# Kernel tuning notes

Measured on AMD Instinct MI355X. Metric: run time of the kernel, lower is better.

## Reference

```python
import jax, jax.numpy as jnp
import numpy as np

NT = 32          # nt_states
T = 64           # t_states
ST = NT + T      # total states
NEG = -1e9       # matches self.huge fill


def setup_inputs() -> dict:
    key = jax.random.key(0)
    k1, k2, k3 = jax.random.split(key, 3)
    B, n = 8, 28
    return {
        "unary_scores": jax.random.normal(k1, (B, n, T), dtype=jnp.float32),
        "rule_scores": jax.random.normal(k2, (B, NT, ST, ST), dtype=jnp.float32),
        "root_scores": jax.random.normal(k3, (B, NT), dtype=jnp.float32),
    }


def _inside(unary_scores, rule_scores, root_scores):
    # Chart indexed beta[b, width, start, state]; span (s, s+w) lives at [b, w, s].
    # Invalid (state-range) slots hold NEG, so exp() underflows them to exactly 0,
    # reproducing the terminal/nonterminal slice logic of the torch code.
    B, n, _ = unary_scores.shape
    beta = jnp.full((B, n, n, ST), NEG, dtype=unary_scores.dtype)
    beta = beta.at[:, 0, :, NT:].set(unary_scores)  # width-0 diagonal: preterminals

    mrule = rule_scores.max(axis=(2, 3))                    # [B, A]
    erule = jnp.exp(rule_scores - mrule[:, :, None, None])  # [B, A, L, R]

    for w in range(1, n):
        S = n - w                     # number of valid start positions
        k = np.arange(w)              # split offset: u = s + k
        # left child: span (s, s+k) -> width k, start s
        left = beta[:, :w, :S, :]                                  # [B, w, S, ST]
        # right child: span (s+k+1, s+w) -> width w-1-k, start s+k+1
        sr = k[:, None] + 1 + np.arange(S)[None, :]                # [w, S]
        right = beta[:, (w - 1 - k)[:, None], sr, :]               # [B, w, S, ST]

        # stable logsumexp over (k, l, r) via exp-space matmuls
        ml = left.max(-1)                                          # [B, w, S]
        mr = right.max(-1)                                         # [B, w, S]
        M = (ml + mr).max(1)                                       # [B, S]
        el = jnp.exp(left - ml[..., None])
        er = jnp.exp(right - mr[..., None] + (ml + mr - M[:, None, :])[..., None])
        numer = jnp.einsum('bksl,bksr->bslr', el, er)              # [B, S, L, R]
        total = jnp.einsum('bslr,balr->bsa', numer, erule)         # [B, S, A]
        score = jnp.log(total) + M[..., None] + mrule[:, None, :]
        beta = beta.at[:, w, :S, :NT].set(score)

    top = beta[:, n - 1, 0, :NT] + root_scores                     # span (0, n-1)
    return jax.nn.logsumexp(top, axis=1)                           # log Z, [B]


def reference(unary_scores, rule_scores, root_scores):
    return _inside(unary_scores, rule_scores, root_scores)
```

## Files before the change

kernel.cpp:

```cpp
#include <hip/hip_runtime.h>
#include <cstdint>
#include <cstddef>


#define NMAX 28
#define SLOTT 864
#define SLOTN 3456

#define R_ELT 0
#define R_F   1856
#define R_G   5568
#define R_F2  9280
#define R_G2  12992
#define R_TRI 16704
#define R_BMX 22736
#define R_ENA 23520
#define C_TRI 0
#define C_BMX 6032
#define C_GPP 6816
#define C_ELK 7584
#define C_ERK 8608
#define C_NUM 14752
#define C_RED 16536
#define LDSF  27616

__device__ __forceinline__ int off32(int w, int n) {
    return (w - 1) * n - (w * (w - 1)) / 2;
}
__device__ __forceinline__ float gload(const float* p) {
    return __hip_atomic_load(p, __ATOMIC_RELAXED, __HIP_MEMORY_SCOPE_AGENT);
}
__device__ __forceinline__ void gstore(float* p, float v) {
    __hip_atomic_store(p, v, __ATOMIC_RELAXED, __HIP_MEMORY_SCOPE_AGENT);
}
__device__ __forceinline__ unsigned gloadu(const unsigned* p) {
    return __hip_atomic_load(p, __ATOMIC_RELAXED, __HIP_MEMORY_SCOPE_AGENT);
}
__device__ __forceinline__ void gstoreu(unsigned* p, unsigned v) {
    __hip_atomic_store(p, v, __ATOMIC_RELAXED, __HIP_MEMORY_SCOPE_AGENT);
}
__device__ __forceinline__ float dot4acc(float4 m, float4 t, float acc) {
    return fmaf(m.x, t.x, fmaf(m.y, t.y, fmaf(m.z, t.z, fmaf(m.w, t.w, acc))));
}
__device__ __forceinline__ float b2f(unsigned short u) {
    return __uint_as_float(((unsigned)u) << 16);
}
__device__ __forceinline__ unsigned short f2b(float x) {
    unsigned u = __float_as_uint(x);
    return (unsigned short)((u + 0x7fffu + ((u >> 16) & 1u)) >> 16);
}
__device__ __forceinline__ float maxM(const float* bmx, int w, int s) {
    float M = -3.0e38f;
    for (int k = 0; k < w; ++k)
        M = fmaxf(M, bmx[k * NMAX + s] + bmx[(w - 1 - k) * NMAX + s + k + 1]);
    return M;
}
__device__ __forceinline__ float maxMc(const float* bmx, int w, int s) {
    float M = -3.0e38f;
    for (int k = 2; k <= w - 3; ++k)
        M = fmaxf(M, bmx[k * NMAX + s] + bmx[(w - 1 - k) * NMAX + s + k + 1]);
    return M;
}
__device__ __forceinline__ void finalize_row(float* lds, int triOff, int bmxOff,
                                             const float* slot, int wf, int n,
                                             int tid) {
    int Sp = n - wf;
    if (tid < Sp * 32) {
        int s = tid >> 5, aa = tid & 31;
        float q = gload(slot + s * 32 + aa);
        float m2 = q;
        for (int off = 16; off > 0; off >>= 1)
            m2 = fmaxf(m2, __shfl_xor(m2, off, 32));
        ((unsigned short*)(lds + triOff))[(off32(wf, n) + s) * 32 + aa] = f2b(q / m2);
        if (aa == 0)
            lds[bmxOff + wf * NMAX + s] = __logf(m2) + maxM(lds + bmxOff, wf, s);
    }
}

__global__ __launch_bounds__(256) void prep_kernel(const float* __restrict__ unary,
                                                   float* __restrict__ elT_g,
                                                   float* __restrict__ bmax0_g,
                                                   unsigned* __restrict__ flags,
                                                   int n) {
    int b = blockIdx.x, tid = threadIdx.x;
    if (tid < 16) gstoreu(&flags[b * 32 + tid], (tid >= 8) ? 4u : 0u);
    for (int pos = tid >> 6; pos < n; pos += 4) {
        int t = tid & 63;
        float v = unary[((size_t)(b * n) + pos) * 64 + t];
        float m = v;
        for (int off = 32; off > 0; off >>= 1) m = fmaxf(m, __shfl_xor(m, off, 64));
        elT_g[(size_t)b * 64 * n + t * n + pos] = __expf(v - m);
        if (t == 0) bmax0_g[b * 32 + pos] = m;
    }
}

__global__ __launch_bounds__(256) void pack_kernel(const float* __restrict__ rule,
                                                   const float* __restrict__ elT_g,
                                                   float* __restrict__ H_g,
                                                   float* __restrict__ F_g,
                                                   float* __restrict__ G_g,
                                                   float* __restrict__ ENa_g,
                                                   float* __restrict__ ENc_g,
                                                   int n) {
    extern __shared__ float sl[];
    int b = blockIdx.y, aa = blockIdx.x, tid = threadIdx.x;
    const int ag = aa >> 2, a4 = aa & 3;
    const float4* rs4 = (const float4*)(rule + (size_t)(b * 32 + aa) * 9216);
    for (int i = tid; i < 2304; i += 256) {
        float4 v = rs4[i];
        float4 o;
        o.x = __expf(v.x); o.y = __expf(v.y); o.z = __expf(v.z); o.w = __expf(v.w);
        ((float4*)sl)[i] = o;
    }
    for (int i = tid; i < 64 * n; i += 256)
        sl[9216 + i] = elT_g[(size_t)b * 64 * n + i];
    __syncthreads();
    const float* elt = sl + 9216;
    if (tid < 256) {
        int flat = tid * 4, l = flat >> 5, r = flat & 31;
        float4 o = *(const float4*)(sl + l * 96 + r);
        *(float4*)(ENc_g + ((size_t)(b * 256 + tid) * 32 + aa) * 4) = o;
    }
    for (int i = tid; i < 1024; i += 256)
        ENa_g[((size_t)(b * 8 + ag) * 4096) + a4 * 1024 + i] = sl[(i >> 5) * 96 + (i & 31)];
    for (int i = tid; i < 64 * n; i += 256) {
        int r = i / n, s = i - r * n;
        float acc = 0.f;
        for (int l = 0; l < 64; ++l)
            acc = fmaf(elt[l * n + s], sl[(32 + l) * 96 + 32 + r], acc);
        H_g[(size_t)(b * 8 + ag) * 7424 + (r * 29 + s) * 4 + a4] = acc;
    }
    for (int i = tid; i < 32 * n; i += 256) {
        int r = i / n, s = i - r * n;
        float acc = 0.f;
        for (int l = 0; l < 64; ++l)
            acc = fmaf(elt[l * n + s], sl[(32 + l) * 96 + r], acc);
        F_g[(size_t)(b * 8 + ag) * 3712 + (r * 29 + s) * 4 + a4] = acc;
    }
    for (int i = tid; i < 32 * n; i += 256) {
        int l = i / n, s = i - l * n;
        float acc = 0.f;
        for (int r = 0; r < 64; ++r)
            acc = fmaf(elt[r * n + s], sl[l * 96 + 32 + r], acc);
        G_g[(size_t)(b * 8 + ag) * 3712 + (l * 29 + s) * 4 + a4] = acc;
    }
}

__global__ __launch_bounds__(1024, 1) void inside_kernel(
    const float* __restrict__ elT_g, const float* __restrict__ bmax0_g,
    const float* __restrict__ H_g, const float* __restrict__ F_g,
    const float* __restrict__ G_g, const float* __restrict__ ENa_g,
    const float* __restrict__ ENc_g,
    float* __restrict__ ringT, float* __restrict__ ringN,
    const float* __restrict__ root, float* __restrict__ out,
    unsigned* __restrict__ flags, int n) {
    extern __shared__ float lds[];
    const int b = blockIdx.x >> 4, ch = blockIdx.x & 15;
    const int tid = threadIdx.x;
    unsigned* const fl = flags + b * 32;
    float* const rT = ringT + (size_t)b * 8 * SLOTT;
    float* const rN = ringN + (size_t)b * 4 * SLOTN;

    if (ch < 8) {
        for (int i = tid; i < 64 * n; i += 1024) {
            int t = i / n, pos = i - t * n;
            lds[R_ELT + t * 29 + pos] = elT_g[(size_t)b * 64 * n + i];
        }
        for (int i = tid; i < 3712; i += 1024) lds[R_F + i] = F_g[(size_t)(b * 8 + ch) * 3712 + i];
        for (int i = tid; i < 3712; i += 1024) lds[R_G + i] = G_g[(size_t)(b * 8 + ch) * 3712 + i];
        for (int i = tid; i < 7424; i += 1024) lds[R_F2 + i] = H_g[(size_t)(b * 8 + ch) * 7424 + i];
        for (int i = tid; i < 4096; i += 1024) lds[R_ENA + i] = ENa_g[(size_t)(b * 8 + ch) * 4096 + i];
        if (tid < n) lds[R_BMX + tid] = bmax0_g[b * 32 + tid];
        __syncthreads();

        for (int w = 1; w < n; ++w) {
            const int S = n - w;
            if (tid < 64) {
                unsigned tgt = 0u;
                if (tid < 8) tgt = (w >= 2) ? (unsigned)(w - 1) : 0u;
                else if (tid < 16 && w >= 5) {
                    int p = (tid - 8) >> 2;
                    if (p == (w & 1)) tgt = (unsigned)w;
                }
                for (;;) {
                    unsigned v = (tid < 16) ? gloadu(&fl[tid]) : 0u;
                    if (__ballot(v < tgt) == 0ull) break;
                    __builtin_amdgcn_s_sleep(1);
                }
            }
            __syncthreads();

            if (w >= 2)
                finalize_row(lds, R_TRI, R_BMX, rT + (size_t)((w - 1) & 7) * SLOTT,
                             w - 1, n, tid);
            __syncthreads();

            if (w == 2) {
                const unsigned short* tri = (const unsigned short*)(lds + R_TRI);
                const int b1 = off32(1, n);
                for (int i = tid; i < 32 * 29 * 4; i += 1024) {
                    int a4 = i & 3, rest = i >> 2, s = rest % 29, rl = rest / 29;
                    if (s < n - 1) {
                        float accF = 0.f, accG = 0.f;
                        for (int q = 0; q < 32; ++q) {
                            float e1 = b2f(tri[(b1 + s) * 32 + q]);
                            accF = fmaf(e1, lds[R_ENA + a4 * 1024 + q * 32 + rl], accF);
                            accG = fmaf(lds[R_ENA + a4 * 1024 + rl * 32 + q], e1, accG);
                        }
                        lds[R_F2 + (rl * 29 + s) * 4 + a4] = accF;
                        lds[R_G2 + (rl * 29 + s) * 4 + a4] = accG;
                    }
                }
                __syncthreads();
            }

            if (tid < S * 4) {
                int s = tid >> 2, a4 = tid & 3, a = ch * 4 + a4;
                float cr0 = 0.f, cr1 = 0.f, cr2 = 0.f, cr3 = 0.f;
                if (w >= 5) {
                    const float* p = rN + (size_t)(w & 3) * SLOTN + (size_t)(s * 32 + a) * 4;
                    cr0 = gload(p); cr1 = gload(p + 1); cr2 = gload(p + 2); cr3 = gload(p + 3);
                }
                float M = maxM(lds + R_BMX, w, s);
                const unsigned short* tri = (const unsigned short*)(lds + R_TRI);
                float t2;
                if (w == 1) {
                    float acc = 0.f;
                    for (int r = 0; r < 64; ++r)
                        acc = fmaf(lds[R_ELT + r * 29 + s + 1],
                                   lds[R_F2 + (r * 29 + s) * 4 + a4], acc);
                    t2 = acc;
                } else {
                    int b1 = off32(w - 1, n);
                    float aTN = 0.f, aNT = 0.f;
                    for (int r = 0; r < 32; ++r)
                        aTN = fmaf(b2f(tri[(b1 + s + 1) * 32 + r]),
                                   lds[R_F + (r * 29 + s) * 4 + a4], aTN);
                    for (int l = 0; l < 32; ++l)
                        aNT = fmaf(b2f(tri[(b1 + s) * 32 + l]),
                                   lds[R_G + (l * 29 + s + w) * 4 + a4], aNT);
                    float g0 = __expf(lds[R_BMX + s] + lds[R_BMX + (w - 1) * NMAX + s + 1] - M);
                    float gw = __expf(lds[R_BMX + (w - 1) * NMAX + s] + lds[R_BMX + s + w] - M);
                    t2 = aTN * g0 + aNT * gw;
                    if (w >= 3) {
                        int b2 = off32(w - 2, n);
                        float e1 = 0.f;
                        for (int r = 0; r < 32; ++r)
                            e1 = fmaf(b2f(tri[(b2 + s + 2) * 32 + r]),
                                      lds[R_F2 + (r * 29 + s) * 4 + a4], e1);
                        t2 = fmaf(e1, __expf(lds[R_BMX + NMAX + s] +
                                             lds[R_BMX + (w - 2) * NMAX + s + 2] - M), t2);
                        if (w >= 4) {
                            float e2 = 0.f;
                            for (int l = 0; l < 32; ++l)
                                e2 = fmaf(b2f(tri[(b2 + s) * 32 + l]),
                                          lds[R_G2 + (l * 29 + s + w - 1) * 4 + a4], e2);
                            t2 = fmaf(e2, __expf(lds[R_BMX + (w - 2) * NMAX + s] +
                                                 lds[R_BMX + NMAX + s + w - 1] - M), t2);
                        }
                    }
                    if (w >= 5) {
                        float Mc = maxMc(lds + R_BMX, w, s);
                        t2 = fmaf(((cr0 + cr1) + (cr2 + cr3)), __expf(Mc - M), t2);
                    }
                }
                gstore(rT + (size_t)(w & 7) * SLOTT + s * 32 + a, t2);
            }
            __syncthreads();
            if (tid == 0) gstoreu(&fl[ch], (unsigned)w);
        }

        if (ch == 0) {
            if (tid < 64) {
                unsigned tgt = (unsigned)(n - 1);
                for (;;) {
                    unsigned v = (tid < 8) ? gloadu(&fl[tid]) : tgt;
                    if (__ballot(v < tgt) == 0ull) break;
                    __builtin_amdgcn_s_sleep(1);
                }
            }
            __syncthreads();
            if (tid < 32) {
                float q = gload(rT + (size_t)((n - 1) & 7) * SLOTT + tid);
                float v = q * __expf(root[b * 32 + tid]);
                for (int off = 16; off > 0; off >>= 1) v += __shfl_xor(v, off, 32);
                if (tid == 0) out[b] = maxM(lds + R_BMX, n - 1, 0) + __logf(v);
            }
        }
    } else {
        const int idx = ch - 8, slice = idx & 3, par = idx >> 2;
        float4 e4;
        {
            int g = tid >> 5, a = tid & 31;
            e4 = *(const float4*)(ENc_g + ((size_t)(b * 256 + slice * 32 + g) * 32 + a) * 4);
        }
        if (tid < n) lds[C_BMX + tid] = bmax0_g[b * 32 + tid];
        __syncthreads();
        int lastFin = 0;
        const int W0 = (par == 1) ? 5 : 6;
        for (int W = W0; W < n; W += 2) {
            const int S = n - W, Sp2 = S | 1;
            const int cnt = W - 4;
            int q4 = (cnt + 3) >> 2; if (!(q4 & 1)) ++q4;
            const int K4 = 4 * q4;
            if (tid < 64) {
                unsigned tgt = (unsigned)(W - 3);
                for (;;) {
                    unsigned v = (tid < 8) ? gloadu(&fl[tid]) : tgt;
                    if (__ballot(v < tgt) == 0ull) break;
                    __builtin_amdgcn_s_sleep(1);
                }
            }
            __syncthreads();
            for (int wf = lastFin + 1; wf <= W - 3; ++wf) {
                finalize_row(lds, C_TRI, C_BMX, rT + (size_t)(wf & 7) * SLOTT, wf, n, tid);
                __syncthreads();
            }
            lastFin = W - 3;
            if (tid < cnt * 32) {
                int k = (tid >> 5) + 2, s = tid & 31;
                if (s < S) {
                    float Mc = maxMc(lds + C_BMX, W, s);
                    lds[C_GPP + (k - 2) * 32 + s] =
                        __expf(lds[C_BMX + k * NMAX + s] +
                               lds[C_BMX + (W - 1 - k) * NMAX + s + k + 1] - Mc);
                }
            }
            __syncthreads();
            if (tid < S * 32) {
                int s = tid >> 5, sym = tid & 31;
                const unsigned short* tri = (const unsigned short*)(lds + C_TRI);
                int eo = (sym * Sp2 + s) * K4;
                for (int k = 2; k <= W - 3; ++k)
                    lds[C_ERK + eo + k - 2] =
                        b2f(tri[(off32(W - 1 - k, n) + s + k + 1) * 32 + sym]) *
                        lds[C_GPP + (k - 2) * 32 + s];
                for (int j = cnt; j < K4; ++j) lds[C_ERK + eo + j] = 0.f;
                if (sym < 4) {
                    int lo = (sym * Sp2 + s) * K4;
                    int gl = slice * 4 + sym;
                    for (int k = 2; k <= W - 3; ++k)
                        lds[C_ELK + lo + k - 2] = b2f(tri[(off32(k, n) + s) * 32 + gl]);
                    for (int j = cnt; j < K4; ++j) lds[C_ELK + lo + j] = 0.f;
                }
            }
            __syncthreads();
            {
                int cL = tid & 127, sh = tid >> 7;
                int lloc = cL >> 5, r = cL & 31;
                unsigned short* np = (unsigned short*)(lds + C_NUM);
                for (int s = sh; s < S; s += 8) {
                    const float* ep = lds + C_ELK + (lloc * Sp2 + s) * K4;
                    const float* rp = lds + C_ERK + (r * Sp2 + s) * K4;
                    float acc = 0.f;
                    for (int j = 0; j < K4; j += 4)
                        acc = dot4acc(*(const float4*)(ep + j), *(const float4*)(rp + j), acc);
                    np[s * 132 + cL] = f2b(acc);
                }
            }
            __syncthreads();
            {
                const unsigned short* np = (const unsigned short*)(lds + C_NUM);
                unsigned short* red = (unsigned short*)(lds + C_RED);
                int g = tid >> 5, a = tid & 31, wv = tid >> 6;
                bool low = (tid & 32) == 0;
                for (int s = 0; s < S; ++s) {
                    const unsigned short* pp = np + s * 132 + g * 4;
                    float acc = b2f(pp[0]) * e4.x + b2f(pp[1]) * e4.y +
                                b2f(pp[2]) * e4.z + b2f(pp[3]) * e4.w;
                    acc += __shfl_xor(acc, 32, 64);
                    if (low) red[wv * 896 + s * 32 + a] = f2b(acc);
                }
            }
            __syncthreads();
            if (tid < S * 32) {
                const unsigned short* red = (const unsigned short*)(lds + C_RED);
                float t = 0.f;
                for (int g2 = 0; g2 < 16; ++g2) t += b2f(red[g2 * 896 + tid]);
                gstore(rN + (size_t)(W & 3) * SLOTN + (size_t)tid * 4 + slice, t);
            }
            __syncthreads();
            if (tid == 0) gstoreu(&fl[ch], (unsigned)W);
        }
    }
}

extern "C" void kernel_launch(void* const* d_in, const int* in_sizes, int n_in,
                              void* d_out, int out_size, void* d_ws, size_t ws_size,
                              hipStream_t stream) {
    const float* unary = (const float*)d_in[0];
    const float* rule  = (const float*)d_in[1];
    const float* root  = (const float*)d_in[2];
    float* out = (float*)d_out;

    const int B = in_sizes[2] / 32;
    int n = in_sizes[0] / (B * 64);

    float* ws = (float*)d_ws;
    float* elT_g = ws;
    float* bmax0 = elT_g + (size_t)B * 64 * n;
    float* H_g   = bmax0 + (size_t)B * 32;
    float* F_g   = H_g + (size_t)B * 8 * 7424;
    float* G_g   = F_g + (size_t)B * 8 * 3712;
    float* ENa_g = G_g + (size_t)B * 8 * 3712;
    float* ENc_g = ENa_g + (size_t)B * 8 * 4096;
    float* ringT = ENc_g + (size_t)B * 32768;
    float* ringN = ringT + (size_t)B * 8 * SLOTT;
    unsigned* flags = (unsigned*)(ringN + (size_t)B * 4 * SLOTN);

    prep_kernel<<<dim3(B), 256, 0, stream>>>(unary, elT_g, bmax0, flags, n);

    const int packLds = (9216 + 64 * n) * 4;
    hipFuncSetAttribute((const void*)pack_kernel,
                        hipFuncAttributeMaxDynamicSharedMemorySize, packLds);
    pack_kernel<<<dim3(32, B), 256, packLds, stream>>>(rule, elT_g, H_g, F_g,
                                                       G_g, ENa_g, ENc_g, n);

    hipFuncSetAttribute((const void*)inside_kernel,
                        hipFuncAttributeMaxDynamicSharedMemorySize, LDSF * 4);
    void* args[] = {
        (void*)&elT_g, (void*)&bmax0, (void*)&H_g, (void*)&F_g, (void*)&G_g,
        (void*)&ENa_g, (void*)&ENc_g, (void*)&ringT, (void*)&ringN,
        (void*)&root, (void*)&out, (void*)&flags, (void*)&n
    };
    hipLaunchCooperativeKernel((void*)inside_kernel, dim3(B * 16), dim3(1024),
                               args, LDSF * 4, stream);
}
```

Measured before the change: 260.8 us.

## Restructure inside pass into row worker plus eight table/contraction blocks per batch

Reorganizes the persistent cooperative kernel from 16 blocks per batch to 9. One row worker block computes each chart row from precomputed per-split folded rule tables for the four outermost split pairs on each side. The other blocks build those tables and compute the central splits' contraction in fp32 LDS instead of bf16. The pack kernel now precomputes the width-1 row and the F/G terminal tables directly, and the row worker prefetches central-split partials from a ring buffer. The aim is to cut per-row synchronization latency on the serial critical path, at the cost of more global table traffic, a larger LDS footprint and a more complex flag protocol.

```diff
diff --git a/kernel.cpp b/kernel.cpp
--- a/kernel.cpp
+++ b/kernel.cpp
@@ -4,25 +4,20 @@
 
 
 #define NMAX 28
-#define SLOTT 864
-#define SLOTN 3456
-
-#define R_ELT 0
-#define R_F   1856
-#define R_G   5568
-#define R_F2  9280
-#define R_G2  12992
-#define R_TRI 16704
-#define R_BMX 22736
-#define R_ENA 23520
-#define C_TRI 0
-#define C_BMX 6032
-#define C_GPP 6816
-#define C_ELK 7584
-#define C_ERK 8608
-#define C_NUM 14752
-#define C_RED 16536
-#define LDSF  27616
+#define RT_SLOT 896
+#define RN_SLOT 1728
+#define TABSZ 28672
+
+#define RW_TRI 0
+#define RW_BMX 12096
+#define RW_CB  12880
+#define CO_TRI 0
+#define CO_BMX 12096
+#define CO_ELK 12880
+#define CO_ERK 16144
+#define CO_NUM 22672
+#define CO_RED 28132
+#define LDSF   35300
 
 __device__ __forceinline__ int off32(int w, int n) {
     return (w - 1) * n - (w * (w - 1)) / 2;
@@ -38,9 +33,6 @@
 }
 __device__ __forceinline__ void gstoreu(unsigned* p, unsigned v) {
     __hip_atomic_store(p, v, __ATOMIC_RELAXED, __HIP_MEMORY_SCOPE_AGENT);
-}
-__device__ __forceinline__ float dot4acc(float4 m, float4 t, float acc) {
-    return fmaf(m.x, t.x, fmaf(m.y, t.y, fmaf(m.z, t.z, fmaf(m.w, t.w, acc))));
 }
 __device__ __forceinline__ float b2f(unsigned short u) {
     return __uint_as_float(((unsigned)u) << 16);
@@ -55,26 +47,22 @@
         M = fmaxf(M, bmx[k * NMAX + s] + bmx[(w - 1 - k) * NMAX + s + k + 1]);
     return M;
 }
-__device__ __forceinline__ float maxMc(const float* bmx, int w, int s) {
+__device__ __forceinline__ float maxMc4(const float* bmx, int w, int s) {
     float M = -3.0e38f;
-    for (int k = 2; k <= w - 3; ++k)
+    for (int k = 4; k <= w - 5; ++k)
         M = fmaxf(M, bmx[k * NMAX + s] + bmx[(w - 1 - k) * NMAX + s + k + 1]);
     return M;
 }
-__device__ __forceinline__ void finalize_row(float* lds, int triOff, int bmxOff,
-                                             const float* slot, int wf, int n,
-                                             int tid) {
-    int Sp = n - wf;
-    if (tid < Sp * 32) {
-        int s = tid >> 5, aa = tid & 31;
-        float q = gload(slot + s * 32 + aa);
-        float m2 = q;
-        for (int off = 16; off > 0; off >>= 1)
-            m2 = fmaxf(m2, __shfl_xor(m2, off, 32));
-        ((unsigned short*)(lds + triOff))[(off32(wf, n) + s) * 32 + aa] = f2b(q / m2);
-        if (aa == 0)
-            lds[bmxOff + wf * NMAX + s] = __logf(m2) + maxM(lds + bmxOff, wf, s);
-    }
+__device__ __forceinline__ float dot32(const float* tri, const float* tab) {
+    float acc = 0.f;
+    #pragma unroll
+    for (int j = 0; j < 8; ++j) {
+        float4 tv = *(const float4*)(tri + j * 4);
+        float4 fv = *(const float4*)(tab + j * 4);
+        acc = fmaf(tv.x, fv.x, acc); acc = fmaf(tv.y, fv.y, acc);
+        acc = fmaf(tv.z, fv.z, acc); acc = fmaf(tv.w, fv.w, acc);
+    }
+    return acc;
 }
 
 __global__ __launch_bounds__(256) void prep_kernel(const float* __restrict__ unary,
@@ -83,7 +71,7 @@
                                                    unsigned* __restrict__ flags,
                                                    int n) {
     int b = blockIdx.x, tid = threadIdx.x;
-    if (tid < 16) gstoreu(&flags[b * 32 + tid], (tid >= 8) ? 4u : 0u);
+    if (tid < 32) gstoreu(&flags[b * 32 + tid], 0u);
     for (int pos = tid >> 6; pos < n; pos += 4) {
         int t = tid & 63;
         float v = unary[((size_t)(b * n) + pos) * 64 + t];
@@ -96,15 +84,15 @@
 
 __global__ __launch_bounds__(256) void pack_kernel(const float* __restrict__ rule,
                                                    const float* __restrict__ elT_g,
-                                                   float* __restrict__ H_g,
-                                                   float* __restrict__ F_g,
-                                                   float* __restrict__ G_g,
+                                                   float* __restrict__ T1_g,
+                                                   float* __restrict__ Ftab,
+                                                   float* __restrict__ Gtab,
                                                    float* __restrict__ ENa_g,
+                                                   float* __restrict__ ENb_g,
                                                    float* __restrict__ ENc_g,
                                                    int n) {
-    extern __shared__ float sl[];
+    __shared__ float sl[11008];
     int b = blockIdx.y, aa = blockIdx.x, tid = threadIdx.x;
-    const int ag = aa >> 2, a4 = aa & 3;
     const float4* rs4 = (const float4*)(rule + (size_t)(b * 32 + aa) * 9216);
     for (int i = tid; i < 2304; i += 256) {
         float4 v = rs4[i];
@@ -116,271 +104,330 @@
         sl[9216 + i] = elT_g[(size_t)b * 64 * n + i];
     __syncthreads();
     const float* elt = sl + 9216;
+    if (tid < (n - 1) * 8) {
+        int s = tid >> 3, sub = tid & 7;
+        float acc = 0.f;
+        for (int l = sub * 8; l < sub * 8 + 8; ++l) {
+            float el = elt[l * n + s];
+            const float* row = sl + (32 + l) * 96 + 32;
+            float inner = 0.f;
+            for (int r = 0; r < 64; ++r)
+                inner = fmaf(elt[r * n + s + 1], row[r], inner);
+            acc = fmaf(el, inner, acc);
+        }
+        acc += __shfl_xor(acc, 1, 8);
+        acc += __shfl_xor(acc, 2, 8);
+        acc += __shfl_xor(acc, 4, 8);
+        if (sub == 0) T1_g[(size_t)b * 864 + s * 32 + aa] = acc;
+    }
+    for (int i = tid; i < 32 * n; i += 256) {
+        int r = i & 31, s = i >> 5;
+        float acc = 0.f;
+        for (int l = 0; l < 64; ++l)
+            acc = fmaf(elt[l * n + s], sl[(32 + l) * 96 + r], acc);
+        Ftab[(size_t)b * TABSZ + (s * 32 + aa) * 32 + r] = acc;
+    }
+    for (int i = tid; i < 32 * n; i += 256) {
+        int l = i & 31, s = i >> 5;
+        float acc = 0.f;
+        for (int r = 0; r < 64; ++r)
+            acc = fmaf(elt[r * n + s], sl[l * 96 + 32 + r], acc);
+        Gtab[(size_t)b * TABSZ + (s * 32 + aa) * 32 + l] = acc;
+    }
+    for (int i = tid; i < 1024; i += 256) {
+        ENa_g[(size_t)b * 32768 + aa * 1024 + i] = sl[(i >> 5) * 96 + (i & 31)];
+        ENb_g[(size_t)b * 32768 + aa * 1024 + i] = sl[(i & 31) * 96 + (i >> 5)];
+    }
     if (tid < 256) {
         int flat = tid * 4, l = flat >> 5, r = flat & 31;
         float4 o = *(const float4*)(sl + l * 96 + r);
         *(float4*)(ENc_g + ((size_t)(b * 256 + tid) * 32 + aa) * 4) = o;
     }
-    for (int i = tid; i < 1024; i += 256)
-        ENa_g[((size_t)(b * 8 + ag) * 4096) + a4 * 1024 + i] = sl[(i >> 5) * 96 + (i & 31)];
-    for (int i = tid; i < 64 * n; i += 256) {
-        int r = i / n, s = i - r * n;
-        float acc = 0.f;
-        for (int l = 0; l < 64; ++l)
-            acc = fmaf(elt[l * n + s], sl[(32 + l) * 96 + 32 + r], acc);
-        H_g[(size_t)(b * 8 + ag) * 7424 + (r * 29 + s) * 4 + a4] = acc;
-    }
-    for (int i = tid; i < 32 * n; i += 256) {
-        int r = i / n, s = i - r * n;
-        float acc = 0.f;
-        for (int l = 0; l < 64; ++l)
-            acc = fmaf(elt[l * n + s], sl[(32 + l) * 96 + r], acc);
-        F_g[(size_t)(b * 8 + ag) * 3712 + (r * 29 + s) * 4 + a4] = acc;
-    }
-    for (int i = tid; i < 32 * n; i += 256) {
-        int l = i / n, s = i - l * n;
-        float acc = 0.f;
-        for (int r = 0; r < 64; ++r)
-            acc = fmaf(elt[r * n + s], sl[l * 96 + 32 + r], acc);
-        G_g[(size_t)(b * 8 + ag) * 3712 + (l * 29 + s) * 4 + a4] = acc;
-    }
 }
 
 __global__ __launch_bounds__(1024, 1) void inside_kernel(
-    const float* __restrict__ elT_g, const float* __restrict__ bmax0_g,
-    const float* __restrict__ H_g, const float* __restrict__ F_g,
-    const float* __restrict__ G_g, const float* __restrict__ ENa_g,
-    const float* __restrict__ ENc_g,
+    const float* __restrict__ T1_g, const float* __restrict__ bmax0_g,
+    float* __restrict__ tabs, const float* __restrict__ ENa_g,
+    const float* __restrict__ ENb_g, const float* __restrict__ ENc_g,
     float* __restrict__ ringT, float* __restrict__ ringN,
     const float* __restrict__ root, float* __restrict__ out,
-    unsigned* __restrict__ flags, int n) {
+    unsigned* __restrict__ flags, int n, int B) {
     extern __shared__ float lds[];
-    const int b = blockIdx.x >> 4, ch = blockIdx.x & 15;
+    const int b = blockIdx.x / 9, r9 = blockIdx.x % 9;
     const int tid = threadIdx.x;
     unsigned* const fl = flags + b * 32;
-    float* const rT = ringT + (size_t)b * 8 * SLOTT;
-    float* const rN = ringN + (size_t)b * 4 * SLOTN;
-
-    if (ch < 8) {
-        for (int i = tid; i < 64 * n; i += 1024) {
-            int t = i / n, pos = i - t * n;
-            lds[R_ELT + t * 29 + pos] = elT_g[(size_t)b * 64 * n + i];
-        }
-        for (int i = tid; i < 3712; i += 1024) lds[R_F + i] = F_g[(size_t)(b * 8 + ch) * 3712 + i];
-        for (int i = tid; i < 3712; i += 1024) lds[R_G + i] = G_g[(size_t)(b * 8 + ch) * 3712 + i];
-        for (int i = tid; i < 7424; i += 1024) lds[R_F2 + i] = H_g[(size_t)(b * 8 + ch) * 7424 + i];
-        for (int i = tid; i < 4096; i += 1024) lds[R_ENA + i] = ENa_g[(size_t)(b * 8 + ch) * 4096 + i];
-        if (tid < n) lds[R_BMX + tid] = bmax0_g[b * 32 + tid];
+    float* const rT = ringT + (size_t)b * 8 * RT_SLOT;
+    float* const rN = ringN + (size_t)b * 4 * RN_SLOT;
+    const size_t tb = (size_t)b * TABSZ;
+    const size_t tstep = (size_t)B * TABSZ;
+
+    if (r9 == 0) {
+        if (tid < n) lds[RW_BMX + tid] = bmax0_g[b * 32 + tid];
         __syncthreads();
 
         for (int w = 1; w < n; ++w) {
             const int S = n - w;
+            if (w >= 3 && w <= 8) {
+                if (tid < 64) {
+                    while (gloadu(fl + 16 + (w - 3)) < 1u)
+                        __builtin_amdgcn_s_sleep(8);
+                }
+                __syncthreads();
+            }
+
+            if (tid < S * 32) {
+                const int s = tid >> 5, a = tid & 31;
+                float Mloc = 0.f, t2;
+                if (w == 1) {
+                    t2 = T1_g[(size_t)b * 864 + tid];
+                    if (a == 0) Mloc = maxM(lds + RW_BMX, 1, s);
+                } else {
+                    float gv = 0.f;
+                    if (a < 9) {
+                        Mloc = maxM(lds + RW_BMX, w, s);
+                        const float* B_ = lds + RW_BMX;
+                        float x = -3.0e38f;
+                        if      (a == 0) x = B_[s] + B_[(w - 1) * NMAX + s + 1];
+                        else if (a == 1) x = B_[(w - 1) * NMAX + s] + B_[s + w];
+                        else if (a == 2 && w >= 3) x = B_[NMAX + s] + B_[(w - 2) * NMAX + s + 2];
+                        else if (a == 3 && w >= 4) x = B_[(w - 2) * NMAX + s] + B_[NMAX + s + w - 1];
+                        else if (a == 4 && w >= 5) x = B_[2 * NMAX + s] + B_[(w - 3) * NMAX + s + 3];
+                        else if (a == 5 && w >= 6) x = B_[(w - 3) * NMAX + s] + B_[2 * NMAX + s + w - 2];
+                        else if (a == 6 && w >= 7) x = B_[3 * NMAX + s] + B_[(w - 4) * NMAX + s + 4];
+                        else if (a == 7 && w >= 8) x = B_[(w - 4) * NMAX + s] + B_[3 * NMAX + s + w - 3];
+                        else if (a == 8 && w >= 9) x = maxMc4(B_, w, s);
+                        gv = (x > -1.0e38f) ? __expf(x - Mloc) : 0.f;
+                    }
+                    float g0 = __shfl(gv, 0, 32), gw = __shfl(gv, 1, 32);
+                    float g1 = __shfl(gv, 2, 32), g2x = __shfl(gv, 3, 32);
+                    float g3 = __shfl(gv, 4, 32), g3x = __shfl(gv, 5, 32);
+                    float g4 = __shfl(gv, 6, 32), g4x = __shfl(gv, 7, 32);
+                    float gc = __shfl(gv, 8, 32);
+                    const float* TRIp = lds + RW_TRI;
+                    const size_t ca = (size_t)(s * 32 + a) * 32;
+                    t2 = g0 * dot32(TRIp + (off32(w - 1, n) + s + 1) * 32,
+                                    tabs + 0 * tstep + tb + ca)
+                       + gw * dot32(TRIp + (off32(w - 1, n) + s) * 32,
+                                    tabs + 1 * tstep + tb + (size_t)((s + w) * 32 + a) * 32);
+                    if (w >= 3)
+                        t2 = fmaf(g1, dot32(TRIp + (off32(w - 2, n) + s + 2) * 32,
+                                            tabs + 2 * tstep + tb + ca), t2);
+                    if (w >= 4)
+                        t2 = fmaf(g2x, dot32(TRIp + (off32(w - 2, n) + s) * 32,
+                                             tabs + 3 * tstep + tb + (size_t)((s + w - 1) * 32 + a) * 32), t2);
+                    if (w >= 5)
+                        t2 = fmaf(g3, dot32(TRIp + (off32(w - 3, n) + s + 3) * 32,
+                                            tabs + 4 * tstep + tb + ca), t2);
+                    if (w >= 6)
+                        t2 = fmaf(g3x, dot32(TRIp + (off32(w - 3, n) + s) * 32,
+                                             tabs + 5 * tstep + tb + (size_t)((s + w - 2) * 32 + a) * 32), t2);
+                    if (w >= 7)
+                        t2 = fmaf(g4, dot32(TRIp + (off32(w - 4, n) + s + 4) * 32,
+                                            tabs + 6 * tstep + tb + ca), t2);
+                    if (w >= 8)
+                        t2 = fmaf(g4x, dot32(TRIp + (off32(w - 4, n) + s) * 32,
+                                             tabs + 7 * tstep + tb + (size_t)((s + w - 3) * 32 + a) * 32), t2);
+                    if (w >= 9)
+                        t2 = fmaf(gc, lds[RW_CB + (w & 1) * 864 + tid], t2);
+                }
+                float m2 = t2;
+                for (int off = 16; off > 0; off >>= 1)
+                    m2 = fmaxf(m2, __shfl_xor(m2, off, 32));
+                float eB = t2 / m2;
+                lds[RW_TRI + (off32(w, n) + s) * 32 + a] = eB;
+                gstore(rT + (size_t)(w & 7) * RT_SLOT + tid, eB);
+                if (a == 0) {
+                    float bm = __logf(m2) + Mloc;
+                    lds[RW_BMX + w * NMAX + s] = bm;
+                    gstore(rT + (size_t)(w & 7) * RT_SLOT + 864 + s, bm);
+                }
+            } else if (tid >= 896) {
+                const int wn = w + 1;
+                if (wn >= 9 && wn < n) {
+                    const int grp = wn & 3, pre = tid - 896;
+                    const unsigned* f0 = fl + 8 + grp * 2;
+                    for (;;) {
+                        if (gloadu(f0) >= (unsigned)wn && gloadu(f0 + 1) >= (unsigned)wn)
+                            break;
+                        __builtin_amdgcn_s_sleep(8);
+                    }
+                    const int Sn = n - wn;
+                    const float* src = rN + (size_t)(wn & 3) * RN_SLOT;
+                    for (int e = pre; e < Sn * 32; e += 128)
+                        lds[RW_CB + (wn & 1) * 864 + e] =
+                            gload(src + e * 2) + gload(src + e * 2 + 1);
+                }
+            }
+            __syncthreads();
+            if (tid == 0) gstoreu(fl, (unsigned)w);
+        }
+
+        if (tid < 32) {
+            float eB = lds[RW_TRI + off32(n - 1, n) * 32 + tid];
+            float v = eB * __expf(root[b * 32 + tid]);
+            for (int off = 16; off > 0; off >>= 1) v += __shfl_xor(v, off, 32);
+            if (tid == 0) out[b] = lds[RW_BMX + (n - 1) * NMAX] + __logf(v);
+        }
+    } else {
+        const int idx = r9 - 1, grp = idx >> 1, sl = idx & 1;
+        int tableId = -1;
+        if (idx == 0) tableId = 0; else if (idx == 1) tableId = 1;
+        else if (idx == 6) tableId = 2; else if (idx == 7) tableId = 3;
+        else if (idx == 4) tableId = 4; else if (idx == 5) tableId = 5;
+
+        if (tableId >= 0) {
+            const int foldRow = 1 + (tableId >> 1);
+            const bool isF = (tableId & 1) == 0;
             if (tid < 64) {
-                unsigned tgt = 0u;
-                if (tid < 8) tgt = (w >= 2) ? (unsigned)(w - 1) : 0u;
-                else if (tid < 16 && w >= 5) {
-                    int p = (tid - 8) >> 2;
-                    if (p == (w & 1)) tgt = (unsigned)w;
-                }
-                for (;;) {
-                    unsigned v = (tid < 16) ? gloadu(&fl[tid]) : 0u;
-                    if (__ballot(v < tgt) == 0ull) break;
-                    __builtin_amdgcn_s_sleep(1);
-                }
-            }
-            __syncthreads();
-
-            if (w >= 2)
-                finalize_row(lds, R_TRI, R_BMX, rT + (size_t)((w - 1) & 7) * SLOTT,
-                             w - 1, n, tid);
-            __syncthreads();
-
-            if (w == 2) {
-                const unsigned short* tri = (const unsigned short*)(lds + R_TRI);
-                const int b1 = off32(1, n);
-                for (int i = tid; i < 32 * 29 * 4; i += 1024) {
-                    int a4 = i & 3, rest = i >> 2, s = rest % 29, rl = rest / 29;
-                    if (s < n - 1) {
-                        float accF = 0.f, accG = 0.f;
-                        for (int q = 0; q < 32; ++q) {
-                            float e1 = b2f(tri[(b1 + s) * 32 + q]);
-                            accF = fmaf(e1, lds[R_ENA + a4 * 1024 + q * 32 + rl], accF);
-                            accG = fmaf(lds[R_ENA + a4 * 1024 + rl * 32 + q], e1, accG);
-                        }
-                        lds[R_F2 + (rl * 29 + s) * 4 + a4] = accF;
-                        lds[R_G2 + (rl * 29 + s) * 4 + a4] = accG;
+                while (gloadu(fl) < (unsigned)foldRow) __builtin_amdgcn_s_sleep(8);
+            }
+            __syncthreads();
+            const int cntE = (n - foldRow) * 32;
+            for (int e = tid; e < cntE; e += 1024)
+                lds[CO_TRI + e] = gload(rT + (size_t)(foldRow & 7) * RT_SLOT + e);
+            __syncthreads();
+            const int maxSx = n - foldRow;
+            if (tid < maxSx * 32) {
+                const int sx = tid >> 5, a = tid & 31;
+                const float* EN = (isF ? ENa_g : ENb_g) + (size_t)b * 32768 + a * 1024;
+                float4 acc[8];
+                #pragma unroll
+                for (int j = 0; j < 8; ++j) acc[j] = make_float4(0.f, 0.f, 0.f, 0.f);
+                for (int q = 0; q < 32; ++q) {
+                    float e = lds[CO_TRI + sx * 32 + q];
+                    const float4* ev = (const float4*)(EN + q * 32);
+                    #pragma unroll
+                    for (int j = 0; j < 8; ++j) {
+                        float4 v = ev[j];
+                        acc[j].x = fmaf(e, v.x, acc[j].x);
+                        acc[j].y = fmaf(e, v.y, acc[j].y);
+                        acc[j].z = fmaf(e, v.z, acc[j].z);
+                        acc[j].w = fmaf(e, v.w, acc[j].w);
                     }
                 }
-                __syncthreads();
-            }
-
-            if (tid < S * 4) {
-                int s = tid >> 2, a4 = tid & 3, a = ch * 4 + a4;
-                float cr0 = 0.f, cr1 = 0.f, cr2 = 0.f, cr3 = 0.f;
-                if (w >= 5) {
-                    const float* p = rN + (size_t)(w & 3) * SLOTN + (size_t)(s * 32 + a) * 4;
-                    cr0 = gload(p); cr1 = gload(p + 1); cr2 = gload(p + 2); cr3 = gload(p + 3);
-                }
-                float M = maxM(lds + R_BMX, w, s);
-                const unsigned short* tri = (const unsigned short*)(lds + R_TRI);
-                float t2;
-                if (w == 1) {
-                    float acc = 0.f;
-                    for (int r = 0; r < 64; ++r)
-                        acc = fmaf(lds[R_ELT + r * 29 + s + 1],
-                                   lds[R_F2 + (r * 29 + s) * 4 + a4], acc);
-                    t2 = acc;
-                } else {
-                    int b1 = off32(w - 1, n);
-                    float aTN = 0.f, aNT = 0.f;
-                    for (int r = 0; r < 32; ++r)
-                        aTN = fmaf(b2f(tri[(b1 + s + 1) * 32 + r]),
-                                   lds[R_F + (r * 29 + s) * 4 + a4], aTN);
-                    for (int l = 0; l < 32; ++l)
-                        aNT = fmaf(b2f(tri[(b1 + s) * 32 + l]),
-                                   lds[R_G + (l * 29 + s + w) * 4 + a4], aNT);
-                    float g0 = __expf(lds[R_BMX + s] + lds[R_BMX + (w - 1) * NMAX + s + 1] - M);
-                    float gw = __expf(lds[R_BMX + (w - 1) * NMAX + s] + lds[R_BMX + s + w] - M);
-                    t2 = aTN * g0 + aNT * gw;
-                    if (w >= 3) {
-                        int b2 = off32(w - 2, n);
-                        float e1 = 0.f;
-                        for (int r = 0; r < 32; ++r)
-                            e1 = fmaf(b2f(tri[(b2 + s + 2) * 32 + r]),
-                                      lds[R_F2 + (r * 29 + s) * 4 + a4], e1);
-                        t2 = fmaf(e1, __expf(lds[R_BMX + NMAX + s] +
-                                             lds[R_BMX + (w - 2) * NMAX + s + 2] - M), t2);
-                        if (w >= 4) {
-                            float e2 = 0.f;
-                            for (int l = 0; l < 32; ++l)
-                                e2 = fmaf(b2f(tri[(b2 + s) * 32 + l]),
-                                          lds[R_G2 + (l * 29 + s + w - 1) * 4 + a4], e2);
-                            t2 = fmaf(e2, __expf(lds[R_BMX + (w - 2) * NMAX + s] +
-                                                 lds[R_BMX + NMAX + s + w - 1] - M), t2);
-                        }
-                    }
-                    if (w >= 5) {
-                        float Mc = maxMc(lds + R_BMX, w, s);
-                        t2 = fmaf(((cr0 + cr1) + (cr2 + cr3)), __expf(Mc - M), t2);
-                    }
-                }
-                gstore(rT + (size_t)(w & 7) * SLOTT + s * 32 + a, t2);
-            }
-            __syncthreads();
-            if (tid == 0) gstoreu(&fl[ch], (unsigned)w);
-        }
-
-        if (ch == 0) {
-            if (tid < 64) {
-                unsigned tgt = (unsigned)(n - 1);
-                for (;;) {
-                    unsigned v = (tid < 8) ? gloadu(&fl[tid]) : tgt;
-                    if (__ballot(v < tgt) == 0ull) break;
-                    __builtin_amdgcn_s_sleep(1);
-                }
-            }
-            __syncthreads();
-            if (tid < 32) {
-                float q = gload(rT + (size_t)((n - 1) & 7) * SLOTT + tid);
-                float v = q * __expf(root[b * 32 + tid]);
-                for (int off = 16; off > 0; off >>= 1) v += __shfl_xor(v, off, 32);
-                if (tid == 0) out[b] = maxM(lds + R_BMX, n - 1, 0) + __logf(v);
-            }
-        }
-    } else {
-        const int idx = ch - 8, slice = idx & 3, par = idx >> 2;
-        float4 e4;
+                float* dp = tabs + (size_t)(2 + tableId) * tstep + tb +
+                            (size_t)(sx * 32 + a) * 32;
+                #pragma unroll
+                for (int j = 0; j < 8; ++j) {
+                    gstore(dp + j * 4 + 0, acc[j].x);
+                    gstore(dp + j * 4 + 1, acc[j].y);
+                    gstore(dp + j * 4 + 2, acc[j].z);
+                    gstore(dp + j * 4 + 3, acc[j].w);
+                }
+            }
+            __syncthreads();
+            if (tid == 0) gstoreu(fl + 16 + tableId, 1u);
+        }
+
+        float4 e4[4];
         {
             int g = tid >> 5, a = tid & 31;
-            e4 = *(const float4*)(ENc_g + ((size_t)(b * 256 + slice * 32 + g) * 32 + a) * 4);
-        }
-        if (tid < n) lds[C_BMX + tid] = bmax0_g[b * 32 + tid];
-        __syncthreads();
-        int lastFin = 0;
-        const int W0 = (par == 1) ? 5 : 6;
-        for (int W = W0; W < n; W += 2) {
+            #pragma unroll
+            for (int i = 0; i < 4; ++i)
+                e4[i] = *(const float4*)(ENc_g +
+                    ((size_t)(b * 256 + sl * 128 + g * 4 + i) * 32 + a) * 4);
+        }
+        int lastFin = 3;
+        const int W0 = (grp == 0) ? 12 : 8 + grp;
+        for (int W = W0; W < n; W += 4) {
             const int S = n - W, Sp2 = S | 1;
-            const int cnt = W - 4;
+            const int cnt = W - 8;
             int q4 = (cnt + 3) >> 2; if (!(q4 & 1)) ++q4;
             const int K4 = 4 * q4;
             if (tid < 64) {
-                unsigned tgt = (unsigned)(W - 3);
-                for (;;) {
-                    unsigned v = (tid < 8) ? gloadu(&fl[tid]) : tgt;
-                    if (__ballot(v < tgt) == 0ull) break;
-                    __builtin_amdgcn_s_sleep(1);
-                }
-            }
-            __syncthreads();
-            for (int wf = lastFin + 1; wf <= W - 3; ++wf) {
-                finalize_row(lds, C_TRI, C_BMX, rT + (size_t)(wf & 7) * SLOTT, wf, n, tid);
-                __syncthreads();
-            }
-            lastFin = W - 3;
-            if (tid < cnt * 32) {
-                int k = (tid >> 5) + 2, s = tid & 31;
-                if (s < S) {
-                    float Mc = maxMc(lds + C_BMX, W, s);
-                    lds[C_GPP + (k - 2) * 32 + s] =
-                        __expf(lds[C_BMX + k * NMAX + s] +
-                               lds[C_BMX + (W - 1 - k) * NMAX + s + k + 1] - Mc);
-                }
+                while (gloadu(fl) < (unsigned)(W - 5)) __builtin_amdgcn_s_sleep(8);
+            }
+            __syncthreads();
+            {
+                const int nf = (W - 5) - lastFin;
+                float ev[4], bv[4];
+                for (int i = 0; i < nf; ++i) {
+                    int wf = lastFin + 1 + i;
+                    ev[i] = (tid < (n - wf) * 32)
+                        ? gload(rT + (size_t)(wf & 7) * RT_SLOT + tid) : 0.f;
+                    bv[i] = (tid < (n - wf))
+                        ? gload(rT + (size_t)(wf & 7) * RT_SLOT + 864 + tid) : 0.f;
+                }
+                for (int i = 0; i < nf; ++i) {
+                    int wf = lastFin + 1 + i;
+                    if (tid < (n - wf) * 32)
+                        lds[CO_TRI + (off32(wf, n) + (tid >> 5)) * 32 + (tid & 31)] = ev[i];
+                    if (tid < (n - wf)) lds[CO_BMX + wf * NMAX + tid] = bv[i];
+                }
+                lastFin = W - 5;
             }
             __syncthreads();
             if (tid < S * 32) {
                 int s = tid >> 5, sym = tid & 31;
-                const unsigned short* tri = (const unsigned short*)(lds + C_TRI);
+                float Mc = maxMc4(lds + CO_BMX, W, s);
                 int eo = (sym * Sp2 + s) * K4;
-                for (int k = 2; k <= W - 3; ++k)
-                    lds[C_ERK + eo + k - 2] =
-                        b2f(tri[(off32(W - 1 - k, n) + s + k + 1) * 32 + sym]) *
-                        lds[C_GPP + (k - 2) * 32 + s];
-                for (int j = cnt; j < K4; ++j) lds[C_ERK + eo + j] = 0.f;
-                if (sym < 4) {
+                for (int k = 4; k <= W - 5; ++k)
+                    lds[CO_ERK + eo + k - 4] =
+                        lds[CO_TRI + (off32(W - 1 - k, n) + s + k + 1) * 32 + sym] *
+                        __expf(lds[CO_BMX + k * NMAX + s] +
+                               lds[CO_BMX + (W - 1 - k) * NMAX + s + k + 1] - Mc);
+                for (int j = cnt; j < K4; ++j) lds[CO_ERK + eo + j] = 0.f;
+                if (sym < 16) {
                     int lo = (sym * Sp2 + s) * K4;
-                    int gl = slice * 4 + sym;
-                    for (int k = 2; k <= W - 3; ++k)
-                        lds[C_ELK + lo + k - 2] = b2f(tri[(off32(k, n) + s) * 32 + gl]);
-                    for (int j = cnt; j < K4; ++j) lds[C_ELK + lo + j] = 0.f;
+                    int gl = sl * 16 + sym;
+                    for (int k = 4; k <= W - 5; ++k)
+                        lds[CO_ELK + lo + k - 4] =
+                            lds[CO_TRI + (off32(k, n) + s) * 32 + gl];
+                    for (int j = cnt; j < K4; ++j) lds[CO_ELK + lo + j] = 0.f;
                 }
             }
             __syncthreads();
             {
-                int cL = tid & 127, sh = tid >> 7;
+                int cL = tid & 511, sh = tid >> 9;
                 int lloc = cL >> 5, r = cL & 31;
-                unsigned short* np = (unsigned short*)(lds + C_NUM);
-                for (int s = sh; s < S; s += 8) {
-                    const float* ep = lds + C_ELK + (lloc * Sp2 + s) * K4;
-                    const float* rp = lds + C_ERK + (r * Sp2 + s) * K4;
+                unsigned short* np = (unsigned short*)(lds + CO_NUM);
+                for (int s = sh; s < S; s += 2) {
+                    const float* ep = lds + CO_ELK + (lloc * Sp2 + s) * K4;
+                    const float* rp = lds + CO_ERK + (r * Sp2 + s) * K4;
                     float acc = 0.f;
-                    for (int j = 0; j < K4; j += 4)
-                        acc = dot4acc(*(const float4*)(ep + j), *(const float4*)(rp + j), acc);
-                    np[s * 132 + cL] = f2b(acc);
+                    for (int j = 0; j < K4; j += 4) {
+                        float4 a4 = *(const float4*)(ep + j);
+                        float4 b4 = *(const float4*)(rp + j);
+                        acc = fmaf(a4.x, b4.x, fmaf(a4.y, b4.y,
+                              fmaf(a4.z, b4.z, fmaf(a4.w, b4.w, acc))));
+                    }
+                    np[s * 520 + cL] = f2b(acc);
                 }
             }
             __syncthreads();
             {
-                const unsigned short* np = (const unsigned short*)(lds + C_NUM);
-                unsigned short* red = (unsigned short*)(lds + C_RED);
+                const char* nbase = (const char*)(lds + CO_NUM);
+                unsigned short* red = (unsigned short*)(lds + CO_RED);
                 int g = tid >> 5, a = tid & 31, wv = tid >> 6;
                 bool low = (tid & 32) == 0;
                 for (int s = 0; s < S; ++s) {
-                    const unsigned short* pp = np + s * 132 + g * 4;
-                    float acc = b2f(pp[0]) * e4.x + b2f(pp[1]) * e4.y +
-                                b2f(pp[2]) * e4.z + b2f(pp[3]) * e4.w;
+                    uint4 u0 = *(const uint4*)(nbase + s * 1040 + g * 32);
+                    uint4 u1 = *(const uint4*)(nbase + s * 1040 + g * 32 + 16);
+                    #define LOu(x) __uint_as_float((x) << 16)
+                    #define HIu(x) __uint_as_float((x) & 0xffff0000u)
+                    float acc = LOu(u0.x) * e4[0].x + HIu(u0.x) * e4[0].y
+                              + LOu(u0.y) * e4[0].z + HIu(u0.y) * e4[0].w
+                              + LOu(u0.z) * e4[1].x + HIu(u0.z) * e4[1].y
+                              + LOu(u0.w) * e4[1].z + HIu(u0.w) * e4[1].w
+                              + LOu(u1.x) * e4[2].x + HIu(u1.x) * e4[2].y
+                              + LOu(u1.y) * e4[2].z + HIu(u1.y) * e4[2].w
+                              + LOu(u1.z) * e4[3].x + HIu(u1.z) * e4[3].y
+                              + LOu(u1.w) * e4[3].z + HIu(u1.w) * e4[3].w;
+                    #undef LOu
+                    #undef HIu
                     acc += __shfl_xor(acc, 32, 64);
                     if (low) red[wv * 896 + s * 32 + a] = f2b(acc);
                 }
             }
             __syncthreads();
             if (tid < S * 32) {
-                const unsigned short* red = (const unsigned short*)(lds + C_RED);
+                const unsigned short* red = (const unsigned short*)(lds + CO_RED);
                 float t = 0.f;
                 for (int g2 = 0; g2 < 16; ++g2) t += b2f(red[g2 * 896 + tid]);
-                gstore(rN + (size_t)(W & 3) * SLOTN + (size_t)tid * 4 + slice, t);
-            }
-            __syncthreads();
-            if (tid == 0) gstoreu(&fl[ch], (unsigned)W);
+                gstore(rN + (size_t)(W & 3) * RN_SLOT + (size_t)tid * 2 + sl, t);
+            }
+            __syncthreads();
+            if (tid == 0) gstoreu(fl + 8 + grp * 2 + sl, (unsigned)W);
         }
     }
 }
@@ -399,30 +446,28 @@
     float* ws = (float*)d_ws;
     float* elT_g = ws;
     float* bmax0 = elT_g + (size_t)B * 64 * n;
-    float* H_g   = bmax0 + (size_t)B * 32;
-    float* F_g   = H_g + (size_t)B * 8 * 7424;
-    float* G_g   = F_g + (size_t)B * 8 * 3712;
-    float* ENa_g = G_g + (size_t)B * 8 * 3712;
-    float* ENc_g = ENa_g + (size_t)B * 8 * 4096;
+    float* T1_g  = bmax0 + (size_t)B * 32;
+    float* tabs  = T1_g + (size_t)B * 864;
+    float* ENa_g = tabs + (size_t)8 * B * TABSZ;
+    float* ENb_g = ENa_g + (size_t)B * 32768;
+    float* ENc_g = ENb_g + (size_t)B * 32768;
     float* ringT = ENc_g + (size_t)B * 32768;
-    float* ringN = ringT + (size_t)B * 8 * SLOTT;
-    unsigned* flags = (unsigned*)(ringN + (size_t)B * 4 * SLOTN);
+    float* ringN = ringT + (size_t)B * 8 * RT_SLOT;
+    unsigned* flags = (unsigned*)(ringN + (size_t)B * 4 * RN_SLOT);
 
     prep_kernel<<<dim3(B), 256, 0, stream>>>(unary, elT_g, bmax0, flags, n);
-
-    const int packLds = (9216 + 64 * n) * 4;
-    hipFuncSetAttribute((const void*)pack_kernel,
-                        hipFuncAttributeMaxDynamicSharedMemorySize, packLds);
-    pack_kernel<<<dim3(32, B), 256, packLds, stream>>>(rule, elT_g, H_g, F_g,
-                                                       G_g, ENa_g, ENc_g, n);
+    pack_kernel<<<dim3(32, B), 256, 0, stream>>>(rule, elT_g, T1_g,
+                                                 tabs + (size_t)0,
+                                                 tabs + (size_t)B * TABSZ,
+                                                 ENa_g, ENb_g, ENc_g, n);
 
     hipFuncSetAttribute((const void*)inside_kernel,
                         hipFuncAttributeMaxDynamicSharedMemorySize, LDSF * 4);
     void* args[] = {
-        (void*)&elT_g, (void*)&bmax0, (void*)&H_g, (void*)&F_g, (void*)&G_g,
-        (void*)&ENa_g, (void*)&ENc_g, (void*)&ringT, (void*)&ringN,
-        (void*)&root, (void*)&out, (void*)&flags, (void*)&n
+        (void*)&T1_g, (void*)&bmax0, (void*)&tabs, (void*)&ENa_g, (void*)&ENb_g,
+        (void*)&ENc_g, (void*)&ringT, (void*)&ringN, (void*)&root, (void*)&out,
+        (void*)&flags, (void*)&n, (void*)&B
     };
-    hipLaunchCooperativeKernel((void*)inside_kernel, dim3(B * 16), dim3(1024),
+    hipLaunchCooperativeKernel((void*)inside_kernel, dim3(B * 9), dim3(1024),
                                args, LDSF * 4, stream);
 }
```

Result: slower. 607.4 us (+132.9%).
